# Kernel optimization log

Measured on AMD Instinct MI355X. Metric: run time of the kernel, lower is better.

Reference implementation:

```python
import jax, jax.numpy as jnp
import numpy as np

NUM_C = 100
DIM_S = 128
SIZE_M = 64
EMB = 128
MAX_CODE_LEN = 128
NODE_COUNT = 10000
PATH_COUNT = 10000
B, L = 16, 128


def setup_inputs() -> dict:
    key = jax.random.key(0)
    ks = jax.random.split(key, 24)
    def nrm(k, shape, fan):
        return jax.random.normal(k, shape, jnp.float32) * np.float32(np.sqrt(2.0 / fan))
    code = jax.random.randint(ks[0], (B, L, NUM_C * 2 + MAX_CODE_LEN * 3), 0, 10000)
    q = jax.random.randint(ks[1], (B, L), 0, NUM_C)
    r = jax.random.randint(ks[2], (B, L), 0, 2 * NUM_C)
    return {
        "code": code, "q": q, "r": r,
        "embed_nodes": nrm(ks[3], (NODE_COUNT + 2, EMB), EMB),
        "embed_paths": nrm(ks[4], (PATH_COUNT + 2, EMB), EMB),
        "W_pt": nrm(ks[5], (3 * EMB, 3 * EMB), 3 * EMB), "b_pt": jnp.zeros((3 * EMB,), jnp.float32),
        "W_att": nrm(ks[6], (3 * EMB, 1), 3 * EMB), "b_att": jnp.zeros((1,), jnp.float32),
        "k_emb": nrm(ks[7], (NUM_C + 1, DIM_S), DIM_S),
        "Mk": nrm(ks[8], (SIZE_M, DIM_S), DIM_S),
        "Mv0": nrm(ks[9], (SIZE_M, DIM_S), DIM_S),
        "v_emb": nrm(ks[10], (NUM_C * 2 + 2, DIM_S), DIM_S),
        "W_e": nrm(ks[11], (4 * DIM_S, DIM_S), 4 * DIM_S), "b_e": jnp.zeros((DIM_S,), jnp.float32),
        "W_a": nrm(ks[12], (4 * DIM_S, DIM_S), 4 * DIM_S), "b_a": jnp.zeros((DIM_S,), jnp.float32),
        "W_f": nrm(ks[13], (2 * DIM_S, DIM_S), 2 * DIM_S), "b_f": jnp.zeros((DIM_S,), jnp.float32),
        "W_p": nrm(ks[14], (DIM_S, 10), DIM_S), "b_p": jnp.zeros((10,), jnp.float32),
    }


def reference(code, q, r, embed_nodes, embed_paths, W_pt, b_pt, W_att, b_att,
              k_emb, Mk, Mv0, v_emb, W_e, b_e, W_a, b_a, W_f, b_f, W_p, b_p):
    bsz = code.shape[0]
    k = k_emb[q]                                    # [B,L,D]
    vr = v_emb[r]                                   # [B,L,D]
    # code2vec path triples: [B,L,MAX_CODE_LEN,3] = (start, path, end)
    c2v = code[:, :, NUM_C * 2:].reshape(bsz, code.shape[1], MAX_CODE_LEN, 3)
    full = jnp.concatenate([embed_nodes[c2v[..., 0]],
                            embed_nodes[c2v[..., 2]],
                            embed_paths[c2v[..., 1]]], axis=3)   # [B,L,P,3E]
    tr = jnp.tanh(full @ W_pt + b_pt)
    cw = tr @ W_att + b_att                          # [B,L,P,1]
    attn = jax.nn.softmax(cw, axis=1)                # faithful: softmax over seq dim (dim=1)
    code_vec = jnp.sum(full * attn, axis=2)          # [B,L,3E]
    v = jnp.concatenate([vr, code_vec], axis=2)      # [B,L,4D]
    w = jax.nn.softmax(k @ Mk.T, axis=-1)            # [B,L,M]
    e = jax.nn.sigmoid(v @ W_e + b_e)                # [B,L,D]
    a = jnp.tanh(v @ W_a + b_a)                      # [B,L,D]
    Mvt0 = jnp.broadcast_to(Mv0, (bsz,) + Mv0.shape) # [B,M,D]

    def step(Mvt, inp):
        et, at, wt = inp                             # [B,D],[B,D],[B,M]
        read = jnp.einsum('bm,bmd->bd', wt, Mvt)     # read pre-update memory (Mv[:, :-1])
        Mvt = Mvt * (1.0 - wt[:, :, None] * et[:, None, :]) + wt[:, :, None] * at[:, None, :]
        return Mvt, read

    _, reads = jax.lax.scan(step, Mvt0,
                            (e.transpose(1, 0, 2), a.transpose(1, 0, 2), w.transpose(1, 0, 2)))
    read = reads.transpose(1, 0, 2)                  # [B,L,D]
    f = jnp.tanh(jnp.concatenate([read, k], axis=-1) @ W_f + b_f)
    # dropout is identity in eval mode
    return jax.nn.sigmoid(f @ W_p + b_p)             # [B,L,10]
```

## Files before the change

kernel.cpp:

```cpp
#include <hip/hip_runtime.h>


typedef unsigned char u8;
typedef unsigned short u16;
typedef unsigned int u32;
typedef unsigned long long u64;
typedef __attribute__((ext_vector_type(8))) short short8;
typedef __attribute__((ext_vector_type(4))) float f32x4;
typedef __attribute__((ext_vector_type(2))) float f32x2;

#define DEV __device__ __forceinline__
#define LOG2E 1.4426950408889634f
#define KSCALE 2.8853900817779268f

DEV u16 f2b(float f) {
    union { float f; u32 i; } v; v.f = f;
    u32 x = v.i;
    u32 r = (x + 0x7FFFu + ((x >> 16) & 1u)) >> 16;
    return (u16)r;
}
DEV u16 f2bt(float f) {
    union { float f; u32 i; } v; v.f = f;
    return (u16)(v.i >> 16);
}
DEV float nexp(float x) { return __builtin_amdgcn_exp2f(x * LOG2E); }
DEV float nrcp(float x) { return __builtin_amdgcn_rcpf(x); }
DEV float fast_tanh(float x) {
    return 1.f - 2.f * nrcp(1.f + __builtin_amdgcn_exp2f(x * (2.f * LOG2E)));
}
DEV float sigmoidf_(float x) { return nrcp(1.f + __builtin_amdgcn_exp2f(-x * LOG2E)); }
DEV f32x2 d8(u32 x, bool hi) {
    return hi ? __builtin_amdgcn_cvt_pk_f32_fp8((int)x, true)
              : __builtin_amdgcn_cvt_pk_f32_fp8((int)x, false);
}
DEV u8 e8(float x) {
    return (u8)(__builtin_amdgcn_cvt_pk_fp8_f32(x, x, 0, false) & 0xFF);
}

__global__ void k_prep(const float* __restrict__ EN, const float* __restrict__ EP,
                       const float* __restrict__ Wpt, const float* __restrict__ bpt,
                       const float* __restrict__ We, const float* __restrict__ Wa,
                       const float* __restrict__ Wf, const float* __restrict__ Wp,
                       const float* __restrict__ Kemb, const float* __restrict__ Mk,
                       u8* __restrict__ EN8, u8* __restrict__ EP8,
                       u16* __restrict__ WeaT, u16* __restrict__ WfT,
                       u16* __restrict__ WpT, float* __restrict__ wsmall,
                       u8* __restrict__ PS8, u8* __restrict__ PE8, u8* __restrict__ PP8) {
    int bid = blockIdx.x;
    if (bid < 2048) {
        const int NEH = 10002 * 64;
        const int T0 = 2 * NEH;
        const int T1 = T0 + 65536;
        const int T2 = T1 + 65536;
        const int T3 = T2 + 32768;
        const int T4 = T3 + 2048;
        for (int i = bid * 256 + threadIdx.x; i < T4; i += 2048 * 256) {
            if (i < NEH) {
                ((u16*)EN8)[i] = (u16)__builtin_amdgcn_cvt_pk_fp8_f32(EN[2 * i], EN[2 * i + 1], 0, false);
            } else if (i < T0) {
                int j = i - NEH;
                ((u16*)EP8)[j] = (u16)__builtin_amdgcn_cvt_pk_fp8_f32(EP[2 * j], EP[2 * j + 1], 0, false);
            } else if (i < T1) {
                int w = i - T0;  int k = w >> 7, n = w & 127;
                WeaT[n * 512 + k] = f2b(We[w]);
            } else if (i < T2) {
                int w = i - T1;  int k = w >> 7, n = w & 127;
                WeaT[(128 + n) * 512 + k] = f2b(Wa[w]);
            } else if (i < T3) {
                int w = i - T2;  int k = w >> 7, n = w & 127;
                WfT[n * 256 + k] = f2b(Wf[w]);
            } else {
                int w = i - T3;  int n = w >> 7, k = w & 127;
                WpT[w] = (n < 10) ? f2b(Wp[k * 10 + n]) : (u16)0;
            }
        }
        return;
    }
    int wv = threadIdx.x >> 6, lane = threadIdx.x & 63;
    if (bid < 2074) {
        int row = (bid - 2048) * 4 + wv;
        if (row >= 101) return;
        float lg = 0.f;
        for (int k = 0; k < 128; k += 8) {
            float mk8[8];
#pragma unroll
            for (int u = 0; u < 8; u++) mk8[u] = Mk[lane * 128 + k + u];
#pragma unroll
            for (int u = 0; u < 8; u++) lg = fmaf(Kemb[row * 128 + k + u], mk8[u], lg);
        }
        float mx = lg;
#pragma unroll
        for (int off = 32; off; off >>= 1) mx = fmaxf(mx, __shfl_xor(mx, off, 64));
        float ex = nexp(lg - mx);
        float sum = ex;
#pragma unroll
        for (int off = 32; off; off >>= 1) sum += __shfl_xor(sum, off, 64);
        wsmall[row * 64 + lane] = ex * nrcp(sum);
        return;
    }
    int pid = bid - 2074;
    int which = pid / 313;
    int r0 = (pid % 313) * 32;
    int m = lane & 15, quad = lane >> 4;
    const float* src = (which == 2) ? EP : EN;
    int koff = which * 128;
    u8* dst = (which == 0) ? PS8 : (which == 1) ? PE8 : PP8;

    short8 a[2][4];
#pragma unroll
    for (int rt = 0; rt < 2; rt++) {
        int row = min(r0 + rt * 16 + m, 10001);
        const float* ab = src + row * 128 + quad * 8;
#pragma unroll
        for (int kc = 0; kc < 4; kc++) {
            float4 f0 = *(const float4*)(ab + kc * 32);
            float4 f1 = *(const float4*)(ab + kc * 32 + 4);
            short8 v;
            v[0] = f2b(f0.x); v[1] = f2b(f0.y); v[2] = f2b(f0.z); v[3] = f2b(f0.w);
            v[4] = f2b(f1.x); v[5] = f2b(f1.y); v[6] = f2b(f1.z); v[7] = f2b(f1.w);
            a[rt][kc] = v;
        }
    }

    for (int nt = 0; nt < 6; nt++) {
        int n0 = wv * 96 + nt * 16;
        int col = n0 + m;
        float bias = (which == 2) ? bpt[col] : 0.f;
        f32x4 acc0 = {0.f, 0.f, 0.f, 0.f};
        f32x4 acc1 = {0.f, 0.f, 0.f, 0.f};
#pragma unroll
        for (int kc = 0; kc < 4; kc++) {
            const float* bb = Wpt + (koff + kc * 32 + quad * 8) * 384 + col;
            short8 bv;
#pragma unroll
            for (int j = 0; j < 8; j++) bv[j] = f2bt(bb[j * 384]);
            acc0 = __builtin_amdgcn_mfma_f32_16x16x32_bf16(a[0][kc], bv, acc0, 0, 0, 0);
            acc1 = __builtin_amdgcn_mfma_f32_16x16x32_bf16(a[1][kc], bv, acc1, 0, 0, 0);
        }
#pragma unroll
        for (int reg = 0; reg < 4; reg++) {
            int row0 = r0 + quad * 4 + reg;
            int row1 = row0 + 16;
            if (row0 < 10002) dst[row0 * 384 + col] = e8((acc0[reg] + bias) * KSCALE);
            if (row1 < 10002) dst[row1 * 384 + col] = e8((acc1[reg] + bias) * KSCALE);
        }
    }
}

__global__ void k_cwsm(const int* __restrict__ code,
                       const u8* __restrict__ PS8, const u8* __restrict__ PE8,
                       const u8* __restrict__ PP8, const float* __restrict__ Watt,
                       float* __restrict__ attn) {
    int bp = blockIdx.x;
    int b = bp >> 7, p = bp & 127;
    int tid = threadIdx.x;
    int g = tid >> 4, gl = tid & 15;
    __shared__ float lgs[128];
    __shared__ float redm[4], reds[4];

    float w24[24];
    const float4* wp = (const float4*)(Watt + gl * 24);
#pragma unroll
    for (int u = 0; u < 6; u++) {
        float4 f = wp[u];
        w24[4 * u + 0] = -2.f * f.x; w24[4 * u + 1] = -2.f * f.y;
        w24[4 * u + 2] = -2.f * f.z; w24[4 * u + 3] = -2.f * f.w;
    }

    int si[8], pi[8], ei[8];
#pragma unroll
    for (int it = 0; it < 8; it++) {
        const int* c = code + ((b * 128 + g + it * 16) * 584 + 200 + 3 * p);
        si[it] = c[0]; pi[it] = c[1]; ei[it] = c[2];
    }

    uint4 cs4, ce4, cq4; uint2 cs2, ce2, cq2;
    {
        const u8* bs = PS8 + si[0] * 384 + gl * 24;
        const u8* be = PE8 + ei[0] * 384 + gl * 24;
        const u8* bq = PP8 + pi[0] * 384 + gl * 24;
        cs4 = *(const uint4*)bs; cs2 = *(const uint2*)(bs + 16);
        ce4 = *(const uint4*)be; ce2 = *(const uint2*)(be + 16);
        cq4 = *(const uint4*)bq; cq2 = *(const uint2*)(bq + 16);
    }
#pragma unroll
    for (int it = 0; it < 8; it++) {
        uint4 ns4, ne4, nq4; uint2 ns2, ne2, nq2;
        if (it < 7) {
            const u8* bs = PS8 + si[it + 1] * 384 + gl * 24;
            const u8* be = PE8 + ei[it + 1] * 384 + gl * 24;
            const u8* bq = PP8 + pi[it + 1] * 384 + gl * 24;
            ns4 = *(const uint4*)bs; ns2 = *(const uint2*)(bs + 16);
            ne4 = *(const uint4*)be; ne2 = *(const uint2*)(be + 16);
            nq4 = *(const uint4*)bq; nq2 = *(const uint2*)(bq + 16);
        }
        u32 sv[6] = { cs4.x, cs4.y, cs4.z, cs4.w, cs2.x, cs2.y };
        u32 ev[6] = { ce4.x, ce4.y, ce4.z, ce4.w, ce2.x, ce2.y };
        u32 qv[6] = { cq4.x, cq4.y, cq4.z, cq4.w, cq2.x, cq2.y };
        float acc = 0.f;
#pragma unroll
        for (int u = 0; u < 6; u++) {
            f32x2 zl = d8(sv[u], false) + d8(ev[u], false) + d8(qv[u], false);
            f32x2 zh = d8(sv[u], true)  + d8(ev[u], true)  + d8(qv[u], true);
            float d0 = 1.f + __builtin_amdgcn_exp2f(zl.x);
            float d1 = 1.f + __builtin_amdgcn_exp2f(zl.y);
            float d2 = 1.f + __builtin_amdgcn_exp2f(zh.x);
            float d3 = 1.f + __builtin_amdgcn_exp2f(zh.y);
            float n01 = fmaf(w24[4 * u + 0], d1, w24[4 * u + 1] * d0);
            float n23 = fmaf(w24[4 * u + 2], d3, w24[4 * u + 3] * d2);
            acc = fmaf(n01, nrcp(d0 * d1), acc);
            acc = fmaf(n23, nrcp(d2 * d3), acc);
        }
        acc += __shfl_xor(acc, 1, 64);
        acc += __shfl_xor(acc, 2, 64);
        acc += __shfl_xor(acc, 4, 64);
        acc += __shfl_xor(acc, 8, 64);
        if (gl == 0) lgs[g + it * 16] = acc;
        if (it < 7) {
            cs4 = ns4; cs2 = ns2;
            ce4 = ne4; ce2 = ne2;
            cq4 = nq4; cq2 = nq2;
        }
    }
    __syncthreads();

    int lane = tid & 63, wvi = tid >> 6;
    float x = (tid < 128) ? lgs[tid] : -1e30f;
    float mx = x;
#pragma unroll
    for (int off = 32; off; off >>= 1) mx = fmaxf(mx, __shfl_xor(mx, off, 64));
    if (lane == 0) redm[wvi] = mx;
    __syncthreads();
    mx = fmaxf(redm[0], redm[1]);
    float ex = nexp(x - mx);
    float sum = ex;
#pragma unroll
    for (int off = 32; off; off >>= 1) sum += __shfl_xor(sum, off, 64);
    if (lane == 0) reds[wvi] = sum;
    __syncthreads();
    float inv = nrcp(reds[0] + reds[1]);
    if (tid < 128) attn[(b * 128 + tid) * 128 + p] = ex * inv;
}

__global__ void k_cvea(const int* __restrict__ code, const float* __restrict__ attn,
                       const u8* __restrict__ EN8, const u8* __restrict__ EP8,
                       const int* __restrict__ rix, const int* __restrict__ qix,
                       const float* __restrict__ Vemb, const float* __restrict__ Kemb,
                       const u16* __restrict__ WeaT,
                       const float* __restrict__ be, const float* __restrict__ ba,
                       float* __restrict__ eb, float* __restrict__ ab,
                       u16* __restrict__ fA) {
    int rt0 = blockIdx.x * 16;
    int tid = threadIdx.x;
    int wv = tid >> 6, lane = tid & 63;
    __shared__ int sip[16][384];
    __shared__ float at[16][128];
    __shared__ u16 vAL[16][520];

    for (int idx = tid; idx < 16 * 384; idx += 256) {
        int r = idx / 384, j = idx - r * 384;
        sip[r][j] = code[(rt0 + r) * 584 + 200 + j];
    }
    for (int idx = tid; idx < 2048; idx += 256) {
        int r = idx >> 7, c = idx & 127;
        at[r][c] = attn[(rt0 + r) * 128 + c];
        vAL[r][c] = f2b(Vemb[rix[rt0 + r] * 128 + c]);
        fA[(rt0 + r) * 256 + 128 + c] = f2b(Kemb[qix[rt0 + r] * 128 + c]);
    }
    __syncthreads();

    int h = lane >> 5, cl = lane & 31;
    int unit = wv * 2 + h;
    int o = cl * 4;
    for (int r = unit; r < 16; r += 8) {
        float a0 = 0.f, a1 = 0.f, a2 = 0.f, a3 = 0.f;
        float b0 = 0.f, b1 = 0.f, b2 = 0.f, b3 = 0.f;
        float c0 = 0.f, c1 = 0.f, c2 = 0.f, c3 = 0.f;
        u32 cur0 = *(const u32*)(EN8 + sip[r][0] * 128 + o);
        u32 cur1 = *(const u32*)(EN8 + sip[r][2] * 128 + o);
        u32 cur2 = *(const u32*)(EP8 + sip[r][1] * 128 + o);
        for (int p = 0; p < 128; p++) {
            u32 n0, n1, n2;
            if (p < 127) {
                n0 = *(const u32*)(EN8 + sip[r][3 * p + 3] * 128 + o);
                n1 = *(const u32*)(EN8 + sip[r][3 * p + 5] * 128 + o);
                n2 = *(const u32*)(EP8 + sip[r][3 * p + 4] * 128 + o);
            }
            float w = at[r][p];
            f32x2 sl = d8(cur0, false), sh = d8(cur0, true);
            f32x2 el = d8(cur1, false), eh = d8(cur1, true);
            f32x2 pl = d8(cur2, false), ph = d8(cur2, true);
            a0 = fmaf(w, sl.x, a0); a1 = fmaf(w, sl.y, a1); a2 = fmaf(w, sh.x, a2); a3 = fmaf(w, sh.y, a3);
            b0 = fmaf(w, el.x, b0); b1 = fmaf(w, el.y, b1); b2 = fmaf(w, eh.x, b2); b3 = fmaf(w, eh.y, b3);
            c0 = fmaf(w, pl.x, c0); c1 = fmaf(w, pl.y, c1); c2 = fmaf(w, ph.x, c2); c3 = fmaf(w, ph.y, c3);
            if (p < 127) { cur0 = n0; cur1 = n1; cur2 = n2; }
        }
        u64 pa = (u64)f2b(a0) | ((u64)f2b(a1) << 16) | ((u64)f2b(a2) << 32) | ((u64)f2b(a3) << 48);
        u64 pb = (u64)f2b(b0) | ((u64)f2b(b1) << 16) | ((u64)f2b(b2) << 32) | ((u64)f2b(b3) << 48);
        u64 pc = (u64)f2b(c0) | ((u64)f2b(c1) << 16) | ((u64)f2b(c2) << 32) | ((u64)f2b(c3) << 48);
        *(u64*)(&vAL[r][128 + o]) = pa;
        *(u64*)(&vAL[r][256 + o]) = pb;
        *(u64*)(&vAL[r][384 + o]) = pc;
    }
    __syncthreads();

    int m = lane & 15, quad = lane >> 4;
#pragma unroll
    for (int cti = 0; cti < 4; cti++) {
        int ct = wv + cti * 4;
        const short8* bp = (const short8*)(WeaT + (ct * 16 + m) * 512 + quad * 8);
        f32x4 acc = {0.f, 0.f, 0.f, 0.f};
#pragma unroll
        for (int kc = 0; kc < 16; kc++) {
            short8 af = *(const short8*)(&vAL[m][kc * 32 + quad * 8]);
            acc = __builtin_amdgcn_mfma_f32_16x16x32_bf16(af, bp[kc * 4], acc, 0, 0, 0);
        }
        int col = ct * 16 + m;
        bool isA = col >= 128;
        int c2 = isA ? col - 128 : col;
        float bias = isA ? ba[c2] : be[c2];
#pragma unroll
        for (int reg = 0; reg < 4; reg++) {
            int row = rt0 + quad * 4 + reg;
            float val = acc[reg] + bias;
            if (isA) ab[row * 128 + c2] = fast_tanh(val);
            else     eb[row * 128 + c2] = sigmoidf_(val);
        }
    }
}

__global__ void k_scan(const float* __restrict__ Mv0, const float* __restrict__ eb,
                       const float* __restrict__ ab, const float* __restrict__ wsmall,
                       const int* __restrict__ qq, u16* __restrict__ fA) {
    int b = blockIdx.x >> 4, dblk = blockIdx.x & 15;
    int lane = threadIdx.x;
    int s = lane >> 3, dlo = lane & 7;
    int d = dblk * 8 + dlo;

    __shared__ float wsm[101 * 64];
    __shared__ float el[128][8];
    __shared__ float al[128][8];
    __shared__ int ql[128];

    for (int i = lane; i < 101 * 64; i += 64) wsm[i] = wsmall[i];
    for (int i = lane; i < 1024; i += 64) {
        int t = i >> 3, dl = i & 7;
        el[t][dl] = eb[(b * 128 + t) * 128 + dblk * 8 + dl];
        al[t][dl] = ab[(b * 128 + t) * 128 + dblk * 8 + dl];
    }
    for (int i = lane; i < 128; i += 64) ql[i] = qq[b * 128 + i];
    __syncthreads();

    float mv[8];
#pragma unroll
    for (int q = 0; q < 8; q++) mv[q] = Mv0[(s * 8 + q) * 128 + d];

    u16* fout = fA + (b * 128) * 256 + d;

    int qt = ql[0];
    const float4* wr = (const float4*)(wsm + qt * 64 + s * 8);
    float4 w0 = wr[0], w1 = wr[1];
    float ecur = el[0][dlo], acur = al[0][dlo];

    for (int t = 0; t < 128; t++) {
        int tn = (t < 127) ? t + 1 : 127;
        int qn = ql[tn];
        const float4* wrn = (const float4*)(wsm + qn * 64 + s * 8);
        float4 nw0 = wrn[0], nw1 = wrn[1];
        float en = el[tn][dlo], an = al[tn][dlo];

        float w[8] = { w0.x, w0.y, w0.z, w0.w, w1.x, w1.y, w1.z, w1.w };
        float rd = 0.f;
#pragma unroll
        for (int q = 0; q < 8; q++) {
            rd = fmaf(w[q], mv[q], rd);
            mv[q] = fmaf(w[q], fmaf(-mv[q], ecur, acur), mv[q]);
        }
        rd += __shfl_xor(rd, 8, 64);
        rd += __shfl_xor(rd, 16, 64);
        rd += __shfl_xor(rd, 32, 64);
        if (s == 0) fout[t * 256] = f2b(rd);

        ecur = en; acur = an; w0 = nw0; w1 = nw1;
    }
}

__global__ void k_outfin(const u16* __restrict__ fA, const u16* __restrict__ WfT,
                         const float* __restrict__ bfp, const u16* __restrict__ WpT,
                         const float* __restrict__ bp, float* __restrict__ out) {
    int rt = blockIdx.x;
    int wv = threadIdx.x >> 6, lane = threadIdx.x & 63;
    int m = lane & 15, quad = lane >> 4;
    __shared__ u16 ftile[16][128];

    const short8* ap = (const short8*)(fA + (rt * 16 + m) * 256 + quad * 8);
    const short8* bpw = (const short8*)(WfT + (wv * 16 + m) * 256 + quad * 8);
    f32x4 acc = {0.f, 0.f, 0.f, 0.f};
#pragma unroll
    for (int kc = 0; kc < 8; kc++)
        acc = __builtin_amdgcn_mfma_f32_16x16x32_bf16(ap[kc * 4], bpw[kc * 4], acc, 0, 0, 0);
    int col = wv * 16 + m;
    float bias = bfp[col];
#pragma unroll
    for (int reg = 0; reg < 4; reg++)
        ftile[quad * 4 + reg][col] = f2b(fast_tanh(acc[reg] + bias));
    __syncthreads();

    if (wv == 0) {
        f32x4 facc = {0.f, 0.f, 0.f, 0.f};
#pragma unroll
        for (int kc = 0; kc < 4; kc++) {
            short8 af = *(const short8*)(&ftile[m][kc * 32 + quad * 8]);
            short8 bf = *(const short8*)(WpT + m * 128 + kc * 32 + quad * 8);
            facc = __builtin_amdgcn_mfma_f32_16x16x32_bf16(af, bf, facc, 0, 0, 0);
        }
        if (m < 10) {
            float bias2 = bp[m];
#pragma unroll
            for (int reg = 0; reg < 4; reg++) {
                int row = rt * 16 + quad * 4 + reg;
                out[row * 10 + m] = sigmoidf_(facc[reg] + bias2);
            }
        }
    }
}

extern "C" void kernel_launch(void* const* d_in, const int* in_sizes, int n_in,
                              void* d_out, int out_size, void* d_ws, size_t ws_size,
                              hipStream_t stream) {
    const int*   code = (const int*)d_in[0];
    const int*   q    = (const int*)d_in[1];
    const int*   r    = (const int*)d_in[2];
    const float* EN   = (const float*)d_in[3];
    const float* EP   = (const float*)d_in[4];
    const float* Wpt  = (const float*)d_in[5];
    const float* bpt  = (const float*)d_in[6];
    const float* Watt = (const float*)d_in[7];
    const float* Kemb = (const float*)d_in[9];
    const float* Mk   = (const float*)d_in[10];
    const float* Mv0  = (const float*)d_in[11];
    const float* Vemb = (const float*)d_in[12];
    const float* We   = (const float*)d_in[13];
    const float* be   = (const float*)d_in[14];
    const float* Wa   = (const float*)d_in[15];
    const float* ba   = (const float*)d_in[16];
    const float* Wf   = (const float*)d_in[17];
    const float* bf_  = (const float*)d_in[18];
    const float* Wp   = (const float*)d_in[19];
    const float* bp   = (const float*)d_in[20];

    char* ws = (char*)d_ws;
    size_t off = 0;
    auto alloc = [&](size_t bytes) { void* p = ws + off; off = (off + bytes + 255) & ~255UL; return p; };
    u8*    PS8    = (u8*)alloc(10002UL * 384);
    u8*    PE8    = (u8*)alloc(10002UL * 384);
    u8*    PP8    = (u8*)alloc(10002UL * 384);
    u8*    EN8    = (u8*)alloc(10002UL * 128);
    u8*    EP8    = (u8*)alloc(10002UL * 128);
    u16*   WeaT   = (u16*)alloc(256UL * 512 * 2);
    u16*   WfT    = (u16*)alloc(128UL * 256 * 2);
    u16*   WpT    = (u16*)alloc(16UL * 128 * 2);
    float* attn   = (float*)alloc(16UL * 128 * 128 * 4);
    u16*   fA     = (u16*)alloc(2048UL * 256 * 2);
    float* eb     = (float*)alloc(2048UL * 128 * 4);
    float* ab     = (float*)alloc(2048UL * 128 * 4);
    float* wsmall = (float*)alloc(101UL * 64 * 4);

    k_prep<<<3013, 256, 0, stream>>>(EN, EP, Wpt, bpt, We, Wa, Wf, Wp, Kemb, Mk,
                                     EN8, EP8, WeaT, WfT, WpT, wsmall, PS8, PE8, PP8);
    k_cwsm<<<2048, 256, 0, stream>>>(code, PS8, PE8, PP8, Watt, attn);
    k_cvea<<<128, 256, 0, stream>>>(code, attn, EN8, EP8, r, q, Vemb, Kemb,
                                    WeaT, be, ba, eb, ab, fA);
    k_scan<<<256, 64, 0, stream>>>(Mv0, eb, ab, wsmall, q, fA);
    k_outfin<<<128, 512, 0, stream>>>(fA, WfT, bf_, WpT, bp, (float*)d_out);
}
```

Measured before the change: 251.8 us.

## Split code-vector gather and e/a GEMM into separate wider-grid kernels

The fused k_cvea kernel, which ran 128 blocks each gathering 16 rows serially over 128 paths, is split into two kernels. k_cv uses one block per row (2048 blocks) and divides the 128 paths across 8 wave-halves, then reduces the partial sums in shared memory. k_eawM runs the e/a MFMA GEMM from a global bf16 vA buffer with 512 blocks, one column tile per wave. This exposes far more parallelism for the latency-bound gather, at the cost of an extra launch and a global round-trip for vA.

```diff
diff --git a/kernel.cpp b/kernel.cpp
--- a/kernel.cpp
+++ b/kernel.cpp
@@ -4,7 +4,6 @@
 typedef unsigned char u8;
 typedef unsigned short u16;
 typedef unsigned int u32;
-typedef unsigned long long u64;
 typedef __attribute__((ext_vector_type(8))) short short8;
 typedef __attribute__((ext_vector_type(4))) float f32x4;
 typedef __attribute__((ext_vector_type(2))) float f32x2;
@@ -242,90 +241,98 @@
     if (tid < 128) attn[(b * 128 + tid) * 128 + p] = ex * inv;
 }
 
-__global__ void k_cvea(const int* __restrict__ code, const float* __restrict__ attn,
-                       const u8* __restrict__ EN8, const u8* __restrict__ EP8,
-                       const int* __restrict__ rix, const int* __restrict__ qix,
-                       const float* __restrict__ Vemb, const float* __restrict__ Kemb,
-                       const u16* __restrict__ WeaT,
-                       const float* __restrict__ be, const float* __restrict__ ba,
-                       float* __restrict__ eb, float* __restrict__ ab,
-                       u16* __restrict__ fA) {
-    int rt0 = blockIdx.x * 16;
+__global__ void k_cv(const int* __restrict__ code, const float* __restrict__ attn,
+                     const u8* __restrict__ EN8, const u8* __restrict__ EP8,
+                     const int* __restrict__ rr, const int* __restrict__ qq,
+                     const float* __restrict__ Vemb, const float* __restrict__ Kemb,
+                     u16* __restrict__ vA, u16* __restrict__ fA) {
+    int row = blockIdx.x;
     int tid = threadIdx.x;
     int wv = tid >> 6, lane = tid & 63;
-    __shared__ int sip[16][384];
-    __shared__ float at[16][128];
-    __shared__ u16 vAL[16][520];
-
-    for (int idx = tid; idx < 16 * 384; idx += 256) {
-        int r = idx / 384, j = idx - r * 384;
-        sip[r][j] = code[(rt0 + r) * 584 + 200 + j];
-    }
-    for (int idx = tid; idx < 2048; idx += 256) {
-        int r = idx >> 7, c = idx & 127;
-        at[r][c] = attn[(rt0 + r) * 128 + c];
-        vAL[r][c] = f2b(Vemb[rix[rt0 + r] * 128 + c]);
-        fA[(rt0 + r) * 256 + 128 + c] = f2b(Kemb[qix[rt0 + r] * 128 + c]);
-    }
-    __syncthreads();
-
     int h = lane >> 5, cl = lane & 31;
-    int unit = wv * 2 + h;
+    __shared__ int si[128], ei[128], pi[128];
+    __shared__ float at[128];
+    __shared__ float part[8][3][128];
+    if (tid < 128) {
+        const int* c = code + (row * 584 + 200);
+        si[tid] = c[3 * tid]; pi[tid] = c[3 * tid + 1]; ei[tid] = c[3 * tid + 2];
+        at[tid] = attn[row * 128 + tid];
+    }
+    if (tid < 128) {
+        vA[row * 512 + tid] = f2b(Vemb[rr[row] * 128 + tid]);
+    } else {
+        int t2 = tid - 128;
+        fA[row * 256 + 128 + t2] = f2b(Kemb[qq[row] * 128 + t2]);
+    }
+    __syncthreads();
+
     int o = cl * 4;
-    for (int r = unit; r < 16; r += 8) {
-        float a0 = 0.f, a1 = 0.f, a2 = 0.f, a3 = 0.f;
-        float b0 = 0.f, b1 = 0.f, b2 = 0.f, b3 = 0.f;
-        float c0 = 0.f, c1 = 0.f, c2 = 0.f, c3 = 0.f;
-        u32 cur0 = *(const u32*)(EN8 + sip[r][0] * 128 + o);
-        u32 cur1 = *(const u32*)(EN8 + sip[r][2] * 128 + o);
-        u32 cur2 = *(const u32*)(EP8 + sip[r][1] * 128 + o);
-        for (int p = 0; p < 128; p++) {
-            u32 n0, n1, n2;
-            if (p < 127) {
-                n0 = *(const u32*)(EN8 + sip[r][3 * p + 3] * 128 + o);
-                n1 = *(const u32*)(EN8 + sip[r][3 * p + 5] * 128 + o);
-                n2 = *(const u32*)(EP8 + sip[r][3 * p + 4] * 128 + o);
-            }
-            float w = at[r][p];
-            f32x2 sl = d8(cur0, false), sh = d8(cur0, true);
-            f32x2 el = d8(cur1, false), eh = d8(cur1, true);
-            f32x2 pl = d8(cur2, false), ph = d8(cur2, true);
-            a0 = fmaf(w, sl.x, a0); a1 = fmaf(w, sl.y, a1); a2 = fmaf(w, sh.x, a2); a3 = fmaf(w, sh.y, a3);
-            b0 = fmaf(w, el.x, b0); b1 = fmaf(w, el.y, b1); b2 = fmaf(w, eh.x, b2); b3 = fmaf(w, eh.y, b3);
-            c0 = fmaf(w, pl.x, c0); c1 = fmaf(w, pl.y, c1); c2 = fmaf(w, ph.x, c2); c3 = fmaf(w, ph.y, c3);
-            if (p < 127) { cur0 = n0; cur1 = n1; cur2 = n2; }
-        }
-        u64 pa = (u64)f2b(a0) | ((u64)f2b(a1) << 16) | ((u64)f2b(a2) << 32) | ((u64)f2b(a3) << 48);
-        u64 pb = (u64)f2b(b0) | ((u64)f2b(b1) << 16) | ((u64)f2b(b2) << 32) | ((u64)f2b(b3) << 48);
-        u64 pc = (u64)f2b(c0) | ((u64)f2b(c1) << 16) | ((u64)f2b(c2) << 32) | ((u64)f2b(c3) << 48);
-        *(u64*)(&vAL[r][128 + o]) = pa;
-        *(u64*)(&vAL[r][256 + o]) = pb;
-        *(u64*)(&vAL[r][384 + o]) = pc;
-    }
-    __syncthreads();
-
+    int pb = wv + h * 4;
+    float a0 = 0.f, a1 = 0.f, a2 = 0.f, a3 = 0.f;
+    float b0 = 0.f, b1 = 0.f, b2 = 0.f, b3 = 0.f;
+    float c0 = 0.f, c1 = 0.f, c2 = 0.f, c3 = 0.f;
+
+    u32 cur0, cur1, cur2;
+    cur0 = *(const u32*)(EN8 + si[pb] * 128 + o);
+    cur1 = *(const u32*)(EN8 + ei[pb] * 128 + o);
+    cur2 = *(const u32*)(EP8 + pi[pb] * 128 + o);
+#pragma unroll
+    for (int it = 0; it < 16; it++) {
+        int p = pb + it * 8;
+        u32 n0, n1, n2;
+        if (it < 15) {
+            int pn = p + 8;
+            n0 = *(const u32*)(EN8 + si[pn] * 128 + o);
+            n1 = *(const u32*)(EN8 + ei[pn] * 128 + o);
+            n2 = *(const u32*)(EP8 + pi[pn] * 128 + o);
+        }
+        float w = at[p];
+        f32x2 sl = d8(cur0, false), sh = d8(cur0, true);
+        f32x2 el = d8(cur1, false), eh = d8(cur1, true);
+        f32x2 pl = d8(cur2, false), ph = d8(cur2, true);
+        a0 = fmaf(w, sl.x, a0); a1 = fmaf(w, sl.y, a1); a2 = fmaf(w, sh.x, a2); a3 = fmaf(w, sh.y, a3);
+        b0 = fmaf(w, el.x, b0); b1 = fmaf(w, el.y, b1); b2 = fmaf(w, eh.x, b2); b3 = fmaf(w, eh.y, b3);
+        c0 = fmaf(w, pl.x, c0); c1 = fmaf(w, pl.y, c1); c2 = fmaf(w, ph.x, c2); c3 = fmaf(w, ph.y, c3);
+        if (it < 15) { cur0 = n0; cur1 = n1; cur2 = n2; }
+    }
+    int slot = wv * 2 + h;
+    part[slot][0][o + 0] = a0; part[slot][0][o + 1] = a1; part[slot][0][o + 2] = a2; part[slot][0][o + 3] = a3;
+    part[slot][1][o + 0] = b0; part[slot][1][o + 1] = b1; part[slot][1][o + 2] = b2; part[slot][1][o + 3] = b3;
+    part[slot][2][o + 0] = c0; part[slot][2][o + 1] = c1; part[slot][2][o + 2] = c2; part[slot][2][o + 3] = c3;
+    __syncthreads();
+    u16* vrow = vA + row * 512 + 128;
+    for (int idx = tid; idx < 384; idx += 256) {
+        int tbl = idx >> 7, col = idx & 127;
+        float s = 0.f;
+#pragma unroll
+        for (int sl2 = 0; sl2 < 8; sl2++) s += part[sl2][tbl][col];
+        vrow[idx] = f2b(s);
+    }
+}
+
+__global__ void k_eawM(const u16* __restrict__ vA, const u16* __restrict__ WeaT,
+                       const float* __restrict__ be, const float* __restrict__ ba,
+                       float* __restrict__ eb, float* __restrict__ ab) {
+    int rt = blockIdx.x >> 2, cg = blockIdx.x & 3;
+    int wv = threadIdx.x >> 6, lane = threadIdx.x & 63;
+    int ct = cg * 4 + wv;
     int m = lane & 15, quad = lane >> 4;
-#pragma unroll
-    for (int cti = 0; cti < 4; cti++) {
-        int ct = wv + cti * 4;
-        const short8* bp = (const short8*)(WeaT + (ct * 16 + m) * 512 + quad * 8);
-        f32x4 acc = {0.f, 0.f, 0.f, 0.f};
-#pragma unroll
-        for (int kc = 0; kc < 16; kc++) {
-            short8 af = *(const short8*)(&vAL[m][kc * 32 + quad * 8]);
-            acc = __builtin_amdgcn_mfma_f32_16x16x32_bf16(af, bp[kc * 4], acc, 0, 0, 0);
-        }
-        int col = ct * 16 + m;
-        bool isA = col >= 128;
-        int c2 = isA ? col - 128 : col;
-        float bias = isA ? ba[c2] : be[c2];
-#pragma unroll
-        for (int reg = 0; reg < 4; reg++) {
-            int row = rt0 + quad * 4 + reg;
-            float val = acc[reg] + bias;
-            if (isA) ab[row * 128 + c2] = fast_tanh(val);
-            else     eb[row * 128 + c2] = sigmoidf_(val);
-        }
+    const short8* ap = (const short8*)(vA + (rt * 16 + m) * 512 + quad * 8);
+    const short8* bp = (const short8*)(WeaT + (ct * 16 + m) * 512 + quad * 8);
+    f32x4 acc = {0.f, 0.f, 0.f, 0.f};
+#pragma unroll
+    for (int kc = 0; kc < 16; kc++)
+        acc = __builtin_amdgcn_mfma_f32_16x16x32_bf16(ap[kc * 4], bp[kc * 4], acc, 0, 0, 0);
+    int col = ct * 16 + m;
+    bool isA = col >= 128;
+    int c2 = isA ? col - 128 : col;
+    float bias = isA ? ba[c2] : be[c2];
+#pragma unroll
+    for (int reg = 0; reg < 4; reg++) {
+        int row = rt * 16 + quad * 4 + reg;
+        float val = acc[reg] + bias;
+        if (isA) ab[row * 128 + c2] = fast_tanh(val);
+        else     eb[row * 128 + c2] = sigmoidf_(val);
     }
 }
 
@@ -461,6 +468,7 @@
     u16*   WfT    = (u16*)alloc(128UL * 256 * 2);
     u16*   WpT    = (u16*)alloc(16UL * 128 * 2);
     float* attn   = (float*)alloc(16UL * 128 * 128 * 4);
+    u16*   vA     = (u16*)alloc(2048UL * 512 * 2);
     u16*   fA     = (u16*)alloc(2048UL * 256 * 2);
     float* eb     = (float*)alloc(2048UL * 128 * 4);
     float* ab     = (float*)alloc(2048UL * 128 * 4);
@@ -469,8 +477,8 @@
     k_prep<<<3013, 256, 0, stream>>>(EN, EP, Wpt, bpt, We, Wa, Wf, Wp, Kemb, Mk,
                                      EN8, EP8, WeaT, WfT, WpT, wsmall, PS8, PE8, PP8);
     k_cwsm<<<2048, 256, 0, stream>>>(code, PS8, PE8, PP8, Watt, attn);
-    k_cvea<<<128, 256, 0, stream>>>(code, attn, EN8, EP8, r, q, Vemb, Kemb,
-                                    WeaT, be, ba, eb, ab, fA);
+    k_cv<<<2048, 256, 0, stream>>>(code, attn, EN8, EP8, r, q, Vemb, Kemb, vA, fA);
+    k_eawM<<<512, 256, 0, stream>>>(vA, WeaT, be, ba, eb, ab);
     k_scan<<<256, 64, 0, stream>>>(Mv0, eb, ab, wsmall, q, fA);
     k_outfin<<<128, 512, 0, stream>>>(fA, WfT, bf_, WpT, bp, (float*)d_out);
 }
```

Result: faster. 222.2 us (-11.8%).
